# Performance work log

Measured on AMD Instinct MI355X. Metric: run time of the kernel, lower is better.

The kernel has to match this reference:

```python
import jax, jax.numpy as jnp
import numpy as np

V, E, H, L, T, B = 50257, 1024, 16, 12, 128, 16
FF = 4 * E
STD = 0.02


def setup_inputs() -> dict:
    key = jax.random.key(0)
    ks = jax.random.split(key, 20)
    n = lambda k, shape: (jax.random.normal(k, shape, dtype=jnp.float32) * STD)
    inp = {
        'idx': jax.random.randint(ks[0], (B, T), 0, V, dtype=jnp.int64),
        'targets': jax.random.randint(ks[1], (B, T), 0, V, dtype=jnp.int64),
        'tok_emb': n(ks[2], (V, E)),
        'pos_emb': n(ks[3], (T, E)),
        'wq': n(ks[4], (L, E, E)),
        'wk': n(ks[5], (L, E, E)),
        'wv': n(ks[6], (L, E, E)),
        'w_proj': n(ks[7], (L, E, E)),
        'b_proj': jnp.zeros((L, E), jnp.float32),
        'ln1_g': jnp.ones((L, E), jnp.float32),
        'ln1_b': jnp.zeros((L, E), jnp.float32),
        'ln2_g': jnp.ones((L, E), jnp.float32),
        'ln2_b': jnp.zeros((L, E), jnp.float32),
        'w_fc1': n(ks[8], (L, E, FF)),
        'b_fc1': jnp.zeros((L, FF), jnp.float32),
        'w_fc2': n(ks[9], (L, FF, E)),
        'b_fc2': jnp.zeros((L, E), jnp.float32),
        'lnf_g': jnp.ones((E,), jnp.float32),
        'lnf_b': jnp.zeros((E,), jnp.float32),
        'w_head': n(ks[10], (E, V)),
        'b_head': jnp.zeros((V,), jnp.float32),
    }
    return inp


def _layernorm(x, g, b, eps=1e-5):
    m = x.mean(-1, keepdims=True)
    v = ((x - m) ** 2).mean(-1, keepdims=True)
    return (x - m) / jnp.sqrt(v + eps) * g + b


def _forward(idx, targets, tok_emb, pos_emb, wq, wk, wv, w_proj, b_proj,
             ln1_g, ln1_b, ln2_g, ln2_b, w_fc1, b_fc1, w_fc2, b_fc2,
             lnf_g, lnf_b, w_head, b_head):
    Bb, Tt = idx.shape
    x = tok_emb[idx] + pos_emb[:Tt]  # (B, T, E)
    causal = jnp.tril(jnp.ones((Tt, Tt), dtype=bool))
    scale = E ** (-0.5)  # NOTE: original scales by full n_embd, not head_size

    def block(x, p):
        (wq_l, wk_l, wv_l, wp_l, bp_l, g1, b1, g2, b2, wf1, bf1, wf2, bf2) = p
        h = _layernorm(x, g1, b1)
        q = (h @ wq_l).reshape(Bb, Tt, H, -1)
        k = (h @ wk_l).reshape(Bb, Tt, H, -1)
        v = (h @ wv_l).reshape(Bb, Tt, H, -1)
        sc = jnp.einsum('bthd,bshd->bhts', q, k) * scale
        sc = jnp.where(causal, sc, -jnp.inf)
        att = jax.nn.softmax(sc, axis=-1)
        o = jnp.einsum('bhts,bshd->bthd', att, v).reshape(Bb, Tt, E)
        x = x + o @ wp_l + bp_l
        h2 = _layernorm(x, g2, b2)
        x = x + jax.nn.relu(h2 @ wf1 + bf1) @ wf2 + bf2
        return x, None

    x, _ = jax.lax.scan(block, x, (wq, wk, wv, w_proj, b_proj, ln1_g, ln1_b,
                                   ln2_g, ln2_b, w_fc1, b_fc1, w_fc2, b_fc2))
    x = _layernorm(x, lnf_g, lnf_b)
    logits = x @ w_head + b_head  # (B, T, V)
    logp = jax.nn.log_softmax(logits, axis=-1)
    nll = -jnp.take_along_axis(logp.reshape(Bb * Tt, -1),
                               targets.reshape(-1, 1), axis=1)
    loss = nll.mean()
    return logits, loss


def reference(idx, targets, tok_emb, pos_emb, wq, wk, wv, w_proj, b_proj,
              ln1_g, ln1_b, ln2_g, ln2_b, w_fc1, b_fc1, w_fc2, b_fc2,
              lnf_g, lnf_b, w_head, b_head):
    return _forward(idx, targets, tok_emb, pos_emb, wq, wk, wv, w_proj, b_proj,
                    ln1_g, ln1_b, ln2_g, ln2_b, w_fc1, b_fc1, w_fc2, b_fc2,
                    lnf_g, lnf_b, w_head, b_head)
```

## Files before the change

### kernel.cpp

```cpp
#include <hip/hip_runtime.h>
#include <math.h>

typedef unsigned short u16;
typedef float f32x4 __attribute__((ext_vector_type(4)));
typedef short bf16x8 __attribute__((ext_vector_type(8)));
typedef unsigned short us4 __attribute__((ext_vector_type(4)));

#define DEVI __device__ __forceinline__

DEVI float bf2f(u16 u) { return __uint_as_float(((unsigned int)u) << 16); }
DEVI u16 f2bf(float f) {
    unsigned int u = __float_as_uint(f);
    u += 0x7fffu + ((u >> 16) & 1u);
    return (u16)(u >> 16);
}

__global__ __launch_bounds__(256) void k_embed(const int* __restrict__ idx,
                                               const float* __restrict__ te,
                                               const float* __restrict__ pe,
                                               float* __restrict__ x) {
    int m = blockIdx.x;
    int t = m & 127;
    int tok = idx[m];
    const f32x4* a = (const f32x4*)(te + (long)tok * 1024);
    const f32x4* p = (const f32x4*)(pe + (long)t * 1024);
    f32x4* o = (f32x4*)(x + (long)m * 1024);
    o[threadIdx.x] = a[threadIdx.x] + p[threadIdx.x];
}

DEVI void ln_body(f32x4 v, const float* g, const float* b, float* red,
                  int tid, int lane, int wid, u16* outrow) {
    float s = v.x + v.y + v.z + v.w;
#pragma unroll
    for (int o2 = 32; o2; o2 >>= 1) s += __shfl_xor(s, o2);
    if (lane == 0) red[wid] = s;
    __syncthreads();
    float mean = (red[0] + red[1] + red[2] + red[3]) * (1.0f / 1024.0f);
    f32x4 d; d.x = v.x - mean; d.y = v.y - mean; d.z = v.z - mean; d.w = v.w - mean;
    float sq = d.x * d.x + d.y * d.y + d.z * d.z + d.w * d.w;
#pragma unroll
    for (int o2 = 32; o2; o2 >>= 1) sq += __shfl_xor(sq, o2);
    if (lane == 0) red[4 + wid] = sq;
    __syncthreads();
    float rstd = rsqrtf((red[4] + red[5] + red[6] + red[7]) * (1.0f / 1024.0f) + 1e-5f);
    f32x4 gg = ((const f32x4*)g)[tid];
    f32x4 bb = ((const f32x4*)b)[tid];
    us4 o4;
    o4.x = f2bf(d.x * rstd * gg.x + bb.x);
    o4.y = f2bf(d.y * rstd * gg.y + bb.y);
    o4.z = f2bf(d.z * rstd * gg.z + bb.z);
    o4.w = f2bf(d.w * rstd * gg.w + bb.w);
    ((us4*)outrow)[tid] = o4;
}

__global__ __launch_bounds__(256) void k_ln(const float* __restrict__ x,
                                            const float* __restrict__ g,
                                            const float* __restrict__ b,
                                            u16* __restrict__ out) {
    __shared__ float red[8];
    int tid = threadIdx.x, lane = tid & 63, wid = tid >> 6;
    int r = blockIdx.x;
    f32x4 v = ((const f32x4*)(x + (long)r * 1024))[tid];
    ln_body(v, g, b, red, tid, lane, wid, out + (long)r * 1024);
}

__global__ __launch_bounds__(256) void k_comb_ln(float* __restrict__ x,
                                                 const float* __restrict__ p01,
                                                 const float* __restrict__ bias,
                                                 const float* __restrict__ g,
                                                 const float* __restrict__ b,
                                                 u16* __restrict__ out) {
    __shared__ float red[8];
    int tid = threadIdx.x, lane = tid & 63, wid = tid >> 6;
    int r = blockIdx.x;
    f32x4 v = ((const f32x4*)(x + (long)r * 1024))[tid];
    f32x4 p0 = ((const f32x4*)(p01 + (long)r * 1024))[tid];
    f32x4 p1 = ((const f32x4*)(p01 + 2048L * 1024 + (long)r * 1024))[tid];
    f32x4 bv = ((const f32x4*)bias)[tid];
    v.x += p0.x + p1.x + bv.x; v.y += p0.y + p1.y + bv.y;
    v.z += p0.z + p1.z + bv.z; v.w += p0.w + p1.w + bv.w;
    ((f32x4*)(x + (long)r * 1024))[tid] = v;
    ln_body(v, g, b, red, tid, lane, wid, out + (long)r * 1024);
}

DEVI void tr_tile(const float* __restrict__ in, u16* __restrict__ out,
                  int K, int N, int k0, int n0, int tid, float (*tile)[65]) {
    int trow = tid >> 4;
    int tcol = (tid & 15) * 4;
#pragma unroll
    for (int p = 0; p < 4; ++p) {
        int k = k0 + trow + p * 16;
        const float* src = in + (long)k * N + n0 + tcol;
#pragma unroll
        for (int j = 0; j < 4; ++j) {
            int n = n0 + tcol + j;
            tile[trow + p * 16][tcol + j] = (n < N) ? src[j] : 0.0f;
        }
    }
    __syncthreads();
#pragma unroll
    for (int p = 0; p < 4; ++p) {
        int n = n0 + trow + p * 16;
        if (n < N) {
            us4 o4;
#pragma unroll
            for (int j = 0; j < 4; ++j) o4[j] = f2bf(tile[tcol + j][trow + p * 16]);
            *(us4*)(out + (long)n * K + k0 + tcol) = o4;
        }
    }
}

__global__ __launch_bounds__(256) void k_tr_one(const float* __restrict__ in,
                                                u16* __restrict__ out, int K, int N) {
    __shared__ float tile[64][65];
    tr_tile(in, out, K, N, blockIdx.y * 64, blockIdx.x * 64, threadIdx.x, tile);
}

__global__ __launch_bounds__(256) void k_tr_layer(
    const float* __restrict__ wq, const float* __restrict__ wk,
    const float* __restrict__ wv, const float* __restrict__ wp,
    const float* __restrict__ f1, const float* __restrict__ f2,
    u16* __restrict__ oqkv, u16* __restrict__ oproj,
    u16* __restrict__ of1, u16* __restrict__ of2) {
    __shared__ float tile[64][65];
    int id = blockIdx.x;
    const float* in; u16* out; int K, N, txx, tyy;
    if (id < 1024) {
        int t = id >> 8, s2 = id & 255;
        txx = s2 & 15; tyy = s2 >> 4; K = 1024; N = 1024;
        in = (t == 0) ? wq : (t == 1) ? wk : (t == 2) ? wv : wp;
        out = (t == 3) ? oproj : oqkv + (long)t * 1024 * 1024;
    } else if (id < 2048) {
        int s2 = id - 1024;
        txx = s2 & 63; tyy = s2 >> 6; K = 1024; N = 4096; in = f1; out = of1;
    } else {
        int s2 = id - 2048;
        txx = s2 & 15; tyy = s2 >> 4; K = 4096; N = 1024; in = f2; out = of2;
    }
    tr_tile(in, out, K, N, tyy * 64, txx * 64, threadIdx.x, tile);
}

template <int ROWS>
DEVI void stage_tile(const u16* __restrict__ g, long row0, long rowmax, int ld,
                     int col0, char* lds, int tid) {
    constexpr int NCH = ROWS * 8;
#pragma unroll
    for (int p = 0; p < NCH / 256; ++p) {
        int c = tid + p * 256;
        int row = c >> 3;
        int gslot = c & 7;
        int gdata = gslot ^ (row & 7);
        long gr = row0 + row;
        if (gr > rowmax) gr = rowmax;
        const u16* src = g + gr * (long)ld + col0 + gdata * 8;
        char* dst = lds + ((long)((tid & 192) + p * 256)) * 16;
        __builtin_amdgcn_global_load_lds(
            (const __attribute__((address_space(1))) void*)src,
            (__attribute__((address_space(3))) void*)dst, 16, 0, 0);
    }
}

template <int ROWS>
DEVI void stage512(const u16* __restrict__ g, long row0, long rowmax, int ld,
                   int col0, char* lds, int tid) {
    constexpr int NP = ROWS * 8 / 512;
#pragma unroll
    for (int p = 0; p < NP; ++p) {
        int c = tid + p * 512;
        int row = c >> 3;
        int gslot = c & 7;
        int gdata = gslot ^ (row & 7);
        long gr = row0 + row;
        if (gr > rowmax) gr = rowmax;
        const u16* src = g + gr * (long)ld + col0 + gdata * 8;
        char* dst = lds + ((long)((tid & 448) + p * 512)) * 16;
        __builtin_amdgcn_global_load_lds(
            (const __attribute__((address_space(1))) void*)src,
            (__attribute__((address_space(3))) void*)dst, 16, 0, 0);
    }
}

template <int BN, bool OUT_BF16, bool RELU, bool HAS_BIAS, bool HAS_RES, bool SPLITK>
__global__ __launch_bounds__(256, 2) void k_gemm(
    const u16* __restrict__ A, const u16* __restrict__ Bt,
    const float* __restrict__ bias, const float* __restrict__ res,
    float* __restrict__ Cf, u16* __restrict__ Cb,
    int M, int N, int K, int ldk, int ldc) {
    constexpr int NR = BN / 32;
    constexpr int ASZ = 128 * 64 * 2;
    constexpr int BSZ = BN * 64 * 2;
    __shared__ __align__(16) char lds[2 * (ASZ + BSZ)];
    int tid = threadIdx.x, lane = tid & 63, wid = tid >> 6;
    int l15 = lane & 15, l4 = lane >> 4;
    int wr = wid >> 1, wc = wid & 1;
    if constexpr (SPLITK) {
        int h = blockIdx.z;
        A += (long)h * K;
        Bt += (long)h * K;
        Cf += (long)h * M * (long)ldc;
    }
    long m0 = (long)blockIdx.y * 128;
    long n0 = (long)blockIdx.x * BN;
    f32x4 acc[4][NR] = {};
    const int nk = K >> 6;

    stage_tile<128>(A, m0, (long)M - 1, ldk, 0, lds, tid);
    stage_tile<BN>(Bt, n0, (long)N - 1, ldk, 0, lds + ASZ, tid);
    int cur = 0;
    for (int kt = 0; kt < nk; ++kt) {
        __syncthreads();
        if (kt + 1 < nk) {
            char* nb = lds + (cur ^ 1) * (ASZ + BSZ);
            stage_tile<128>(A, m0, (long)M - 1, ldk, (kt + 1) << 6, nb, tid);
            stage_tile<BN>(Bt, n0, (long)N - 1, ldk, (kt + 1) << 6, nb + ASZ, tid);
        }
        const char* ab = lds + cur * (ASZ + BSZ);
        const char* bb = ab + ASZ;
#pragma unroll
        for (int kh = 0; kh < 2; ++kh) {
            bf16x8 af[4], bfv[NR];
#pragma unroll
            for (int mi = 0; mi < 4; ++mi) {
                int row = wr * 64 + mi * 16 + l15;
                int slot = (kh * 4 + l4) ^ (row & 7);
                af[mi] = *(const bf16x8*)(ab + (row * 8 + slot) * 16);
            }
#pragma unroll
            for (int ni = 0; ni < NR; ++ni) {
                int row = wc * (BN / 2) + ni * 16 + l15;
                int slot = (kh * 4 + l4) ^ (row & 7);
                bfv[ni] = *(const bf16x8*)(bb + (row * 8 + slot) * 16);
            }
#pragma unroll
            for (int mi = 0; mi < 4; ++mi)
#pragma unroll
                for (int ni = 0; ni < NR; ++ni)
                    acc[mi][ni] = __builtin_amdgcn_mfma_f32_16x16x32_bf16(
                        af[mi], bfv[ni], acc[mi][ni], 0, 0, 0);
        }
        cur ^= 1;
    }
#pragma unroll
    for (int ni = 0; ni < NR; ++ni) {
        long n = n0 + wc * (BN / 2) + ni * 16 + l15;
        if (n < N) {
            float bv = HAS_BIAS ? bias[n] : 0.0f;
#pragma unroll
            for (int mi = 0; mi < 4; ++mi) {
#pragma unroll
                for (int j = 0; j < 4; ++j) {
                    long m = m0 + wr * 64 + mi * 16 + l4 * 4 + j;
                    float v = acc[mi][ni][j] + bv;
                    if (HAS_RES) v += res[m * (long)ldc + n];
                    if (RELU) v = fmaxf(v, 0.0f);
                    if (OUT_BF16) Cb[m * (long)ldc + n] = f2bf(v);
                    else Cf[m * (long)ldc + n] = v;
                }
            }
        }
    }
}

__global__ __launch_bounds__(512, 1) void k_head256(
    const u16* __restrict__ A, const u16* __restrict__ Bt,
    const float* __restrict__ bias, float* __restrict__ Cf,
    float2* __restrict__ part, int M, int N, int K, int ldc) {
    constexpr int ASZ = 256 * 64 * 2;
    constexpr int BSZ = 128 * 64 * 2;
    constexpr int TSZ = ASZ + BSZ;
    __shared__ __align__(16) char lds[3 * TSZ];
    int tid = threadIdx.x, lane = tid & 63, wid = tid >> 6;
    int l15 = lane & 15, l4 = lane >> 4;
    int wr = wid >> 1, wc = wid & 1;
    int bn = blockIdx.x, bm = blockIdx.y;
    long m0 = (long)bm * 256, n0 = (long)bn * 128;
    f32x4 acc[4][4] = {};
    const int nk = K >> 6;

#pragma unroll
    for (int t = 0; t < 3; ++t) {
        char* buf = lds + t * TSZ;
        stage512<256>(A, m0, (long)M - 1, K, t << 6, buf, tid);
        stage512<128>(Bt, n0, (long)N - 1, K, t << 6, buf + ASZ, tid);
    }
    for (int t = 0; t < nk; ++t) {
        if (t + 2 < nk)      asm volatile("s_waitcnt vmcnt(12)" ::: "memory");
        else if (t + 1 < nk) asm volatile("s_waitcnt vmcnt(6)" ::: "memory");
        else                 asm volatile("s_waitcnt vmcnt(0)" ::: "memory");
        __builtin_amdgcn_s_barrier();
        const char* ab = lds + (t % 3) * TSZ;
        const char* bb = ab + ASZ;
#pragma unroll
        for (int kh = 0; kh < 2; ++kh) {
            bf16x8 af[4], bfv[4];
#pragma unroll
            for (int mi = 0; mi < 4; ++mi) {
                int row = wr * 64 + mi * 16 + l15;
                int slot = (kh * 4 + l4) ^ (row & 7);
                af[mi] = *(const bf16x8*)(ab + (row * 8 + slot) * 16);
            }
#pragma unroll
            for (int ni = 0; ni < 4; ++ni) {
                int row = wc * 64 + ni * 16 + l15;
                int slot = (kh * 4 + l4) ^ (row & 7);
                bfv[ni] = *(const bf16x8*)(bb + (row * 8 + slot) * 16);
            }
            __builtin_amdgcn_s_setprio(1);
#pragma unroll
            for (int mi = 0; mi < 4; ++mi)
#pragma unroll
                for (int ni = 0; ni < 4; ++ni)
                    acc[mi][ni] = __builtin_amdgcn_mfma_f32_16x16x32_bf16(
                        af[mi], bfv[ni], acc[mi][ni], 0, 0, 0);
            __builtin_amdgcn_s_setprio(0);
        }
        __builtin_amdgcn_s_barrier();
        if (t + 3 < nk) {
            char* buf = lds + (t % 3) * TSZ;
            stage512<256>(A, m0, (long)M - 1, K, (t + 3) << 6, buf, tid);
            stage512<128>(Bt, n0, (long)N - 1, K, (t + 3) << 6, buf + ASZ, tid);
        }
    }
    const float BIG_NEG = -1e30f;
    float bvv[4];
#pragma unroll
    for (int ni = 0; ni < 4; ++ni) {
        long n = n0 + wc * 64 + ni * 16 + l15;
        bvv[ni] = (n < N) ? bias[n] : 0.0f;
    }
    __syncthreads();
    float* ldsF = (float*)lds;
#pragma unroll
    for (int mi = 0; mi < 4; ++mi)
#pragma unroll
        for (int ni = 0; ni < 4; ++ni)
#pragma unroll
            for (int j = 0; j < 4; ++j) {
                int row = wr * 64 + mi * 16 + l4 * 4 + j;
                int col = wc * 64 + ni * 16 + l15;
                long n = n0 + col;
                float v = acc[mi][ni][j] + bvv[ni];
                if (n >= N) v = BIG_NEG;
                ldsF[row * 129 + col] = v;
            }
    __syncthreads();
#pragma unroll 4
    for (int i = 0; i < 64; ++i) {
        int flat = tid + (i << 9);
        int row = flat >> 7, col = flat & 127;
        long n = n0 + col;
        if (n < N)
            __builtin_nontemporal_store(ldsF[row * 129 + col],
                                        &Cf[(m0 + row) * (long)ldc + n]);
    }
    {
        int r = tid >> 1, half = tid & 1;
        const float* rp = ldsF + r * 129 + half * 64;
        float mx = BIG_NEG;
#pragma unroll 8
        for (int c = 0; c < 64; ++c) mx = fmaxf(mx, rp[c]);
        float sm = 0.f;
#pragma unroll 8
        for (int c = 0; c < 64; ++c) sm += __expf(rp[c] - mx);
        float mo = __shfl_xor(mx, 1), so = __shfl_xor(sm, 1);
        float nm = fmaxf(mx, mo);
        float S = sm * __expf(mx - nm) + so * __expf(mo - nm);
        if (half == 0)
            part[(long)bn * M + m0 + r] = make_float2(nm, S);
    }
}

__global__ __launch_bounds__(256) void k_attn_mfma(const u16* __restrict__ qkv,
                                                   u16* __restrict__ o) {
    __shared__ __align__(16) u16 Ks[128 * 64];
    __shared__ __align__(16) u16 Vt[64 * 128];
    __shared__ __align__(16) u16 Ps[4][32 * 128];
    int tid = threadIdx.x, lane = tid & 63, w = tid >> 6;
    int l15 = lane & 15, l4 = lane >> 4;
    int b = blockIdx.x >> 4, h = blockIdx.x & 15;
    const u16* base = qkv + (long)b * 128 * 3072 + h * 64;

    stage_tile<128>(base + 1024, 0, 127, 3072, 0, (char*)Ks, tid);
    {
        const u16* vg = base + 2048;
#pragma unroll
        for (int p = 0; p < 4; ++p) {
            int s0 = (w * 4 + p) * 8;
            u16 tmp[8];
#pragma unroll
            for (int j = 0; j < 8; ++j) tmp[j] = vg[(long)(s0 + j) * 3072 + lane];
            int slot = (s0 >> 3) ^ (lane & 7);
            *(bf16x8*)((char*)Vt + lane * 256 + slot * 16) = *(bf16x8*)tmp;
        }
    }
    bf16x8 aq[2][2];
#pragma unroll
    for (int mj = 0; mj < 2; ++mj)
#pragma unroll
        for (int kk = 0; kk < 2; ++kk)
            aq[mj][kk] = *(const bf16x8*)(base + (long)(w * 32 + mj * 16 + l15) * 3072 + kk * 32 + l4 * 8);
    __syncthreads();

    f32x4 sacc[2][8] = {};
#pragma unroll
    for (int sj = 0; sj < 8; ++sj) {
        bf16x8 bk[2];
#pragma unroll
        for (int kk = 0; kk < 2; ++kk) {
            int row = sj * 16 + l15;
            int slot = (kk * 4 + l4) ^ (row & 7);
            bk[kk] = *(const bf16x8*)((char*)Ks + (row * 8 + slot) * 16);
        }
#pragma unroll
        for (int mj = 0; mj < 2; ++mj) {
            sacc[mj][sj] = __builtin_amdgcn_mfma_f32_16x16x32_bf16(aq[mj][0], bk[0], sacc[mj][sj], 0, 0, 0);
            sacc[mj][sj] = __builtin_amdgcn_mfma_f32_16x16x32_bf16(aq[mj][1], bk[1], sacc[mj][sj], 0, 0, 0);
        }
    }
    const float scale = 0.03125f;
#pragma unroll
    for (int mj = 0; mj < 2; ++mj) {
#pragma unroll
        for (int j = 0; j < 4; ++j) {
            int tq = w * 32 + mj * 16 + l4 * 4 + j;
            float mx = -INFINITY;
#pragma unroll
            for (int sj = 0; sj < 8; ++sj) {
                int s = sj * 16 + l15;
                float v = (s <= tq) ? sacc[mj][sj][j] * scale : -INFINITY;
                sacc[mj][sj][j] = v;
                mx = fmaxf(mx, v);
            }
#pragma unroll
            for (int ofs = 1; ofs < 16; ofs <<= 1) mx = fmaxf(mx, __shfl_xor(mx, ofs));
            float sm = 0.f;
#pragma unroll
            for (int sj = 0; sj < 8; ++sj) {
                float e = __expf(sacc[mj][sj][j] - mx);
                sacc[mj][sj][j] = e;
                sm += e;
            }
#pragma unroll
            for (int ofs = 1; ofs < 16; ofs <<= 1) sm += __shfl_xor(sm, ofs);
            float inv = 1.0f / sm;
            int m2 = mj * 16 + l4 * 4 + j;
            u16* prow = Ps[w] + m2 * 128;
#pragma unroll
            for (int sj = 0; sj < 8; ++sj) {
                int s = sj * 16 + l15;
                int slot = (s >> 3) ^ (m2 & 7);
                prow[slot * 8 + (s & 7)] = f2bf(sacc[mj][sj][j] * inv);
            }
        }
    }
    f32x4 oacc[2][4] = {};
#pragma unroll
    for (int kk = 0; kk < 4; ++kk) {
        bf16x8 pa[2], bv[4];
#pragma unroll
        for (int mj = 0; mj < 2; ++mj) {
            int m2 = mj * 16 + l15;
            int slot = (kk * 4 + l4) ^ (m2 & 7);
            pa[mj] = *(const bf16x8*)((char*)(Ps[w]) + m2 * 256 + slot * 16);
        }
#pragma unroll
        for (int nb = 0; nb < 4; ++nb) {
            int d = nb * 16 + l15;
            int slot = (kk * 4 + l4) ^ (d & 7);
            bv[nb] = *(const bf16x8*)((char*)Vt + d * 256 + slot * 16);
        }
#pragma unroll
        for (int mj = 0; mj < 2; ++mj)
#pragma unroll
            for (int nb = 0; nb < 4; ++nb)
                oacc[mj][nb] = __builtin_amdgcn_mfma_f32_16x16x32_bf16(pa[mj], bv[nb], oacc[mj][nb], 0, 0, 0);
    }
#pragma unroll
    for (int mj = 0; mj < 2; ++mj)
#pragma unroll
        for (int nb = 0; nb < 4; ++nb) {
            int d = nb * 16 + l15;
#pragma unroll
            for (int j = 0; j < 4; ++j) {
                int tq = w * 32 + mj * 16 + l4 * 4 + j;
                o[((long)b * 128 + tq) * 1024 + h * 64 + d] = f2bf(oacc[mj][nb][j]);
            }
        }
}

__global__ __launch_bounds__(64) void k_loss_rows2(const float2* __restrict__ part,
                                                   const float* __restrict__ logits,
                                                   const int* __restrict__ tgt,
                                                   float* __restrict__ rowloss, int ncb) {
    int r = blockIdx.x, lane = threadIdx.x;
    float M = -1e30f, S = 0.f;
    for (int cb = lane; cb < ncb; cb += 64) {
        float2 p = part[(long)cb * 2048 + r];
        float nm = fmaxf(M, p.x);
        S = S * __expf(M - nm) + p.y * __expf(p.x - nm);
        M = nm;
    }
#pragma unroll
    for (int ofs = 32; ofs; ofs >>= 1) {
        float M2 = __shfl_xor(M, ofs), S2 = __shfl_xor(S, ofs);
        float nm = fmaxf(M, M2);
        S = S * __expf(M - nm) + S2 * __expf(M2 - nm);
        M = nm;
    }
    if (lane == 0)
        rowloss[r] = (M + logf(S)) - logits[(long)r * 50257 + tgt[r]];
}

__global__ __launch_bounds__(256) void k_loss_reduce(const float* __restrict__ rowloss,
                                                     float* __restrict__ out) {
    __shared__ float red[4];
    int tid = threadIdx.x, lane = tid & 63, wid = tid >> 6;
    float s = 0.f;
    for (int i = tid; i < 2048; i += 256) s += rowloss[i];
#pragma unroll
    for (int ofs = 32; ofs; ofs >>= 1) s += __shfl_xor(s, ofs);
    if (lane == 0) red[wid] = s;
    __syncthreads();
    if (tid == 0) out[0] = (red[0] + red[1] + red[2] + red[3]) * (1.0f / 2048.0f);
}

extern "C" void kernel_launch(void* const* d_in, const int* in_sizes, int n_in,
                              void* d_out, int out_size, void* d_ws, size_t ws_size,
                              hipStream_t stream) {
    (void)in_sizes; (void)n_in; (void)out_size; (void)ws_size;
    const int*   idx     = (const int*)d_in[0];
    const int*   targets = (const int*)d_in[1];
    const float* tok_emb = (const float*)d_in[2];
    const float* pos_emb = (const float*)d_in[3];
    const float* wq      = (const float*)d_in[4];
    const float* wk      = (const float*)d_in[5];
    const float* wv      = (const float*)d_in[6];
    const float* w_proj  = (const float*)d_in[7];
    const float* b_proj  = (const float*)d_in[8];
    const float* ln1_g   = (const float*)d_in[9];
    const float* ln1_b   = (const float*)d_in[10];
    const float* ln2_g   = (const float*)d_in[11];
    const float* ln2_b   = (const float*)d_in[12];
    const float* w_fc1   = (const float*)d_in[13];
    const float* b_fc1   = (const float*)d_in[14];
    const float* w_fc2   = (const float*)d_in[15];
    const float* b_fc2   = (const float*)d_in[16];
    const float* lnf_g   = (const float*)d_in[17];
    const float* lnf_b   = (const float*)d_in[18];
    const float* w_head  = (const float*)d_in[19];
    const float* b_head  = (const float*)d_in[20];
    float* out = (float*)d_out;

    char* w = (char*)d_ws;
    auto alloc = [&](size_t bytes) {
        char* p = w;
        w += (bytes + 255) & ~(size_t)255;
        return p;
    };
    u16*    wT_qkv  = (u16*)alloc(3072L * 1024 * 2);
    u16*    wT_proj = (u16*)alloc(1024L * 1024 * 2);
    u16*    wT_f1   = (u16*)alloc(4096L * 1024 * 2);
    u16*    wT_f2   = (u16*)alloc(1024L * 4096 * 2);
    u16*    wT_head = (u16*)alloc(50257L * 1024 * 2);
    float*  x       = (float*)alloc(2048L * 1024 * 4);
    u16*    h_bf    = (u16*)alloc(2048L * 1024 * 2);
    u16*    qkvb    = (u16*)alloc(2048L * 3072 * 2);
    u16*    o_bf    = (u16*)alloc(2048L * 1024 * 2);
    u16*    ff_bf   = (u16*)alloc(2048L * 4096 * 2);
    float*  p01     = (float*)alloc(2L * 2048 * 1024 * 4);
    float2* part    = (float2*)alloc(393L * 2048 * 8);
    float*  rowloss = (float*)alloc(2048L * 4);

    k_embed<<<2048, 256, 0, stream>>>(idx, tok_emb, pos_emb, x);
    k_tr_one<<<dim3(786, 16), 256, 0, stream>>>(w_head, wT_head, 1024, 50257);

    for (int l = 0; l < 12; ++l) {
        k_tr_layer<<<3072, 256, 0, stream>>>(
            wq + (long)l * 1048576, wk + (long)l * 1048576,
            wv + (long)l * 1048576, w_proj + (long)l * 1048576,
            w_fc1 + (long)l * 4194304, w_fc2 + (long)l * 4194304,
            wT_qkv, wT_proj, wT_f1, wT_f2);
        if (l == 0)
            k_ln<<<2048, 256, 0, stream>>>(x, ln1_g, ln1_b, h_bf);
        else
            k_comb_ln<<<2048, 256, 0, stream>>>(x, p01, b_fc2 + (l - 1) * 1024,
                                                ln1_g + l * 1024, ln1_b + l * 1024, h_bf);
        k_gemm<128, true, false, false, false, false><<<dim3(24, 16), 256, 0, stream>>>(
            h_bf, wT_qkv, nullptr, nullptr, nullptr, qkvb, 2048, 3072, 1024, 1024, 3072);
        k_attn_mfma<<<256, 256, 0, stream>>>(qkvb, o_bf);
        k_gemm<64, false, false, true, true, false><<<dim3(16, 16), 256, 0, stream>>>(
            o_bf, wT_proj, b_proj + l * 1024, x, x, nullptr, 2048, 1024, 1024, 1024, 1024);
        k_ln<<<2048, 256, 0, stream>>>(x, ln2_g + l * 1024, ln2_b + l * 1024, h_bf);
        k_gemm<128, true, true, true, false, false><<<dim3(32, 16), 256, 0, stream>>>(
            h_bf, wT_f1, b_fc1 + l * 4096, nullptr, nullptr, ff_bf, 2048, 4096, 1024, 1024, 4096);
        k_gemm<64, false, false, false, false, true><<<dim3(16, 16, 2), 256, 0, stream>>>(
            ff_bf, wT_f2, nullptr, nullptr, p01, nullptr, 2048, 1024, 2048, 4096, 1024);
    }
    k_comb_ln<<<2048, 256, 0, stream>>>(x, p01, b_fc2 + 11 * 1024, lnf_g, lnf_b, h_bf);
    k_head256<<<dim3(393, 8), 512, 0, stream>>>(h_bf, wT_head, b_head, out, part,
                                                2048, 50257, 1024, 50257);
    k_loss_rows2<<<2048, 64, 0, stream>>>(part, out, targets, rowloss, 393);
    k_loss_reduce<<<1, 256, 0, stream>>>(rowloss, out + 102926336L);
}
```

Before: 1.913 ms.

## Shrink head GEMM LDS for higher occupancy and split-K the proj GEMM

The vocab-head GEMM moves from a triple-buffered BK=64 pipeline to a double-buffered BK=32 tile with a new 4-slot swizzle. Its epilogue now runs in two 128-row passes so LDS fits in about 66KB, and launch bounds are raised to allow more resident blocks. Separately, the attention projection GEMM becomes a 2-way split-K that writes partials, which the combine+layernorm kernel folds in along with the residual and bias. The aim is better latency hiding through occupancy and more parallelism in the proj GEMM, at the cost of a shallower prefetch, more barriers per K step, and extra partial-sum traffic.

Result: faster. 1.856 ms (-3.0%).

```diff
diff --git a/kernel.cpp b/kernel.cpp
--- a/kernel.cpp
+++ b/kernel.cpp
@@ -161,15 +161,15 @@
 }
 
 template <int ROWS>
-DEVI void stage512(const u16* __restrict__ g, long row0, long rowmax, int ld,
-                   int col0, char* lds, int tid) {
-    constexpr int NP = ROWS * 8 / 512;
+DEVI void stage32(const u16* __restrict__ g, long row0, long rowmax, int ld,
+                  int col0, char* lds, int tid) {
+    constexpr int NP = ROWS * 4 / 512;
 #pragma unroll
     for (int p = 0; p < NP; ++p) {
         int c = tid + p * 512;
-        int row = c >> 3;
-        int gslot = c & 7;
-        int gdata = gslot ^ (row & 7);
+        int row = c >> 2;
+        int gslot = c & 3;
+        int gdata = gslot ^ (row & 3) ^ ((row >> 2) & 3);
         long gr = row0 + row;
         if (gr > rowmax) gr = rowmax;
         const u16* src = g + gr * (long)ld + col0 + gdata * 8;
@@ -261,65 +261,54 @@
     }
 }
 
-__global__ __launch_bounds__(512, 1) void k_head256(
+__global__ __launch_bounds__(512, 4) void k_head256(
     const u16* __restrict__ A, const u16* __restrict__ Bt,
     const float* __restrict__ bias, float* __restrict__ Cf,
     float2* __restrict__ part, int M, int N, int K, int ldc) {
-    constexpr int ASZ = 256 * 64 * 2;
-    constexpr int BSZ = 128 * 64 * 2;
+    constexpr int ASZ = 256 * 32 * 2;
+    constexpr int BSZ = 128 * 32 * 2;
     constexpr int TSZ = ASZ + BSZ;
-    __shared__ __align__(16) char lds[3 * TSZ];
+    __shared__ __align__(16) char lds[128 * 129 * 4];
     int tid = threadIdx.x, lane = tid & 63, wid = tid >> 6;
     int l15 = lane & 15, l4 = lane >> 4;
     int wr = wid >> 1, wc = wid & 1;
     int bn = blockIdx.x, bm = blockIdx.y;
     long m0 = (long)bm * 256, n0 = (long)bn * 128;
     f32x4 acc[4][4] = {};
-    const int nk = K >> 6;
-
-#pragma unroll
-    for (int t = 0; t < 3; ++t) {
-        char* buf = lds + t * TSZ;
-        stage512<256>(A, m0, (long)M - 1, K, t << 6, buf, tid);
-        stage512<128>(Bt, n0, (long)N - 1, K, t << 6, buf + ASZ, tid);
-    }
-    for (int t = 0; t < nk; ++t) {
-        if (t + 2 < nk)      asm volatile("s_waitcnt vmcnt(12)" ::: "memory");
-        else if (t + 1 < nk) asm volatile("s_waitcnt vmcnt(6)" ::: "memory");
-        else                 asm volatile("s_waitcnt vmcnt(0)" ::: "memory");
-        __builtin_amdgcn_s_barrier();
-        const char* ab = lds + (t % 3) * TSZ;
+    const int nk = K >> 5;
+
+    stage32<256>(A, m0, (long)M - 1, K, 0, lds, tid);
+    stage32<128>(Bt, n0, (long)N - 1, K, 0, lds + ASZ, tid);
+    int cur = 0;
+    for (int kt = 0; kt < nk; ++kt) {
+        __syncthreads();
+        if (kt + 1 < nk) {
+            char* nb = lds + (cur ^ 1) * TSZ;
+            stage32<256>(A, m0, (long)M - 1, K, (kt + 1) << 5, nb, tid);
+            stage32<128>(Bt, n0, (long)N - 1, K, (kt + 1) << 5, nb + ASZ, tid);
+        }
+        const char* ab = lds + cur * TSZ;
         const char* bb = ab + ASZ;
-#pragma unroll
-        for (int kh = 0; kh < 2; ++kh) {
-            bf16x8 af[4], bfv[4];
-#pragma unroll
-            for (int mi = 0; mi < 4; ++mi) {
-                int row = wr * 64 + mi * 16 + l15;
-                int slot = (kh * 4 + l4) ^ (row & 7);
-                af[mi] = *(const bf16x8*)(ab + (row * 8 + slot) * 16);
-            }
-#pragma unroll
-            for (int ni = 0; ni < 4; ++ni) {
-                int row = wc * 64 + ni * 16 + l15;
-                int slot = (kh * 4 + l4) ^ (row & 7);
-                bfv[ni] = *(const bf16x8*)(bb + (row * 8 + slot) * 16);
-            }
-            __builtin_amdgcn_s_setprio(1);
-#pragma unroll
-            for (int mi = 0; mi < 4; ++mi)
-#pragma unroll
-                for (int ni = 0; ni < 4; ++ni)
-                    acc[mi][ni] = __builtin_amdgcn_mfma_f32_16x16x32_bf16(
-                        af[mi], bfv[ni], acc[mi][ni], 0, 0, 0);
-            __builtin_amdgcn_s_setprio(0);
-        }
-        __builtin_amdgcn_s_barrier();
-        if (t + 3 < nk) {
-            char* buf = lds + (t % 3) * TSZ;
-            stage512<256>(A, m0, (long)M - 1, K, (t + 3) << 6, buf, tid);
-            stage512<128>(Bt, n0, (long)N - 1, K, (t + 3) << 6, buf + ASZ, tid);
-        }
+        bf16x8 af[4], bfv[4];
+#pragma unroll
+        for (int mi = 0; mi < 4; ++mi) {
+            int row = wr * 64 + mi * 16 + l15;
+            int slot = (l4 ^ (row & 3) ^ ((row >> 2) & 3)) & 3;
+            af[mi] = *(const bf16x8*)(ab + (row * 4 + slot) * 16);
+        }
+#pragma unroll
+        for (int ni = 0; ni < 4; ++ni) {
+            int row = wc * 64 + ni * 16 + l15;
+            int slot = (l4 ^ (row & 3) ^ ((row >> 2) & 3)) & 3;
+            bfv[ni] = *(const bf16x8*)(bb + (row * 4 + slot) * 16);
+        }
+#pragma unroll
+        for (int mi = 0; mi < 4; ++mi)
+#pragma unroll
+            for (int ni = 0; ni < 4; ++ni)
+                acc[mi][ni] = __builtin_amdgcn_mfma_f32_16x16x32_bf16(
+                    af[mi], bfv[ni], acc[mi][ni], 0, 0, 0);
+        cur ^= 1;
     }
     const float BIG_NEG = -1e30f;
     float bvv[4];
@@ -328,45 +317,51 @@
         long n = n0 + wc * 64 + ni * 16 + l15;
         bvv[ni] = (n < N) ? bias[n] : 0.0f;
     }
-    __syncthreads();
     float* ldsF = (float*)lds;
 #pragma unroll
-    for (int mi = 0; mi < 4; ++mi)
-#pragma unroll
-        for (int ni = 0; ni < 4; ++ni)
-#pragma unroll
-            for (int j = 0; j < 4; ++j) {
-                int row = wr * 64 + mi * 16 + l4 * 4 + j;
-                int col = wc * 64 + ni * 16 + l15;
-                long n = n0 + col;
-                float v = acc[mi][ni][j] + bvv[ni];
-                if (n >= N) v = BIG_NEG;
-                ldsF[row * 129 + col] = v;
-            }
-    __syncthreads();
+    for (int pass = 0; pass < 2; ++pass) {
+        int rbase = pass * 128;
+        __syncthreads();
+        if ((wr >> 1) == pass) {
+#pragma unroll
+            for (int mi = 0; mi < 4; ++mi)
+#pragma unroll
+                for (int ni = 0; ni < 4; ++ni)
+#pragma unroll
+                    for (int j = 0; j < 4; ++j) {
+                        int row = wr * 64 + mi * 16 + l4 * 4 + j - rbase;
+                        int col = wc * 64 + ni * 16 + l15;
+                        long n = n0 + col;
+                        float v = acc[mi][ni][j] + bvv[ni];
+                        if (n >= N) v = BIG_NEG;
+                        ldsF[row * 129 + col] = v;
+                    }
+        }
+        __syncthreads();
 #pragma unroll 4
-    for (int i = 0; i < 64; ++i) {
-        int flat = tid + (i << 9);
-        int row = flat >> 7, col = flat & 127;
-        long n = n0 + col;
-        if (n < N)
-            __builtin_nontemporal_store(ldsF[row * 129 + col],
-                                        &Cf[(m0 + row) * (long)ldc + n]);
-    }
-    {
-        int r = tid >> 1, half = tid & 1;
-        const float* rp = ldsF + r * 129 + half * 64;
-        float mx = BIG_NEG;
+        for (int i = 0; i < 32; ++i) {
+            int flat = tid + (i << 9);
+            int row = flat >> 7, col = flat & 127;
+            long n = n0 + col;
+            if (n < N)
+                __builtin_nontemporal_store(ldsF[row * 129 + col],
+                                            &Cf[(m0 + rbase + row) * (long)ldc + n]);
+        }
+        if (tid < 256) {
+            int r = tid >> 1, half = tid & 1;
+            const float* rp = ldsF + r * 129 + half * 64;
+            float mx = BIG_NEG;
 #pragma unroll 8
-        for (int c = 0; c < 64; ++c) mx = fmaxf(mx, rp[c]);
-        float sm = 0.f;
+            for (int c = 0; c < 64; ++c) mx = fmaxf(mx, rp[c]);
+            float sm = 0.f;
 #pragma unroll 8
-        for (int c = 0; c < 64; ++c) sm += __expf(rp[c] - mx);
-        float mo = __shfl_xor(mx, 1), so = __shfl_xor(sm, 1);
-        float nm = fmaxf(mx, mo);
-        float S = sm * __expf(mx - nm) + so * __expf(mo - nm);
-        if (half == 0)
-            part[(long)bn * M + m0 + r] = make_float2(nm, S);
+            for (int c = 0; c < 64; ++c) sm += __expf(rp[c] - mx);
+            float mo = __shfl_xor(mx, 1), so = __shfl_xor(sm, 1);
+            float nm = fmaxf(mx, mo);
+            float S = sm * __expf(mx - nm) + so * __expf(mo - nm);
+            if (half == 0)
+                part[(long)bn * M + m0 + rbase + r] = make_float2(nm, S);
+        }
     }
 }
 
@@ -588,9 +583,10 @@
         k_gemm<128, true, false, false, false, false><<<dim3(24, 16), 256, 0, stream>>>(
             h_bf, wT_qkv, nullptr, nullptr, nullptr, qkvb, 2048, 3072, 1024, 1024, 3072);
         k_attn_mfma<<<256, 256, 0, stream>>>(qkvb, o_bf);
-        k_gemm<64, false, false, true, true, false><<<dim3(16, 16), 256, 0, stream>>>(
-            o_bf, wT_proj, b_proj + l * 1024, x, x, nullptr, 2048, 1024, 1024, 1024, 1024);
-        k_ln<<<2048, 256, 0, stream>>>(x, ln2_g + l * 1024, ln2_b + l * 1024, h_bf);
+        k_gemm<64, false, false, false, false, true><<<dim3(16, 16, 2), 256, 0, stream>>>(
+            o_bf, wT_proj, nullptr, nullptr, p01, nullptr, 2048, 1024, 512, 1024, 1024);
+        k_comb_ln<<<2048, 256, 0, stream>>>(x, p01, b_proj + l * 1024,
+                                            ln2_g + l * 1024, ln2_b + l * 1024, h_bf);
         k_gemm<128, true, true, true, false, false><<<dim3(32, 16), 256, 0, stream>>>(
             h_bf, wT_f1, b_fc1 + l * 4096, nullptr, nullptr, ff_bf, 2048, 4096, 1024, 1024, 4096);
         k_gemm<64, false, false, false, false, true><<<dim3(16, 16, 2), 256, 0, stream>>>(
```
